# Performance work log

Measured on AMD Instinct MI355X. Metric: run time of the kernel, lower is better.

The kernel has to match this reference:

```python
import jax, jax.numpy as jnp
import numpy as np

T, B, D = 2048, 4, 1024

def setup_inputs() -> dict:
    key = jax.random.key(0)
    ks = jax.random.split(key, 4)
    return {
        "query": jax.random.normal(ks[0], (T, B, D), jnp.float32),
        "input_feature": jax.random.normal(ks[1], (T, B, D), jnp.float32),
        "in_proj_weight": jax.random.normal(ks[2], (2 * D, D), jnp.float32) * (D ** -0.5),
        "in_proj_bias": jnp.zeros((2 * D,), jnp.float32),
        "out_proj_weight": jax.random.normal(ks[3], (D, D), jnp.float32) * (D ** -0.5),
        "out_proj_bias": jnp.zeros((D,), jnp.float32),
    }

def reference(query, input_feature, in_proj_weight, in_proj_bias, out_proj_weight, out_proj_bias):
    d = query.shape[-1]
    scaling = d ** -0.5
    # joint KV projection: [T,B,2D], then chunk
    kv = jnp.einsum('tbd,ed->tbe', input_feature, in_proj_weight) + in_proj_bias
    k, v = kv[..., :d], kv[..., d:]
    q = query * scaling
    # attn_weights: [B, T(query), S(key)]
    attn_weights = jnp.einsum('tbd,sbd->bts', q, k)
    attn_weights = jax.nn.softmax(attn_weights.astype(jnp.float32), axis=-1).astype(q.dtype)
    # attn: [B,T,D] -> [T,B,D]
    attn = jnp.einsum('bts,sbd->tbd', attn_weights, v)
    attn = jnp.einsum('tbd,ed->tbe', attn, out_proj_weight) + out_proj_bias
    return attn, attn_weights
```

## Files before the change

### kernel.cpp

```cpp
#include <hip/hip_runtime.h>
#include <hip/hip_bf16.h>
#include <type_traits>

static constexpr int T = 2048;
static constexpr int B = 4;
static constexpr int D = 1024;
static constexpr int E = 2 * D;
static constexpr int M1 = T * B;

typedef __attribute__((ext_vector_type(8))) short short8;
typedef __attribute__((ext_vector_type(4))) float f32x4;

__device__ inline ushort f2bf(float x) {
    __hip_bfloat16 h = __float2bfloat16(x);
    return __builtin_bit_cast(ushort, h);
}

__device__ inline void glds16(const void* g, void* l) {
    __builtin_amdgcn_global_load_lds(
        (const __attribute__((address_space(1))) void*)g,
        (__attribute__((address_space(3))) void*)l, 16, 0, 0);
}

template <typename OT>
__global__ __launch_bounds__(256) void mfma_gemm_nt(
    const ushort* __restrict__ A, const ushort* __restrict__ Bt,
    OT* __restrict__ C, const float* __restrict__ bias,
    int K, int lda, int ldb, int ldc,
    long long aBatch, long long bBatch, long long cBatch, float alpha)
{
    __shared__ ushort As[128 * 64];
    __shared__ ushort Bs[128 * 64];

    const int tid  = threadIdx.x;
    const int lane = tid & 63;
    const int wave = tid >> 6;
    const int wm = (wave & 1) * 64;
    const int wn = (wave >> 1) * 64;

    const int bm = blockIdx.y * 128;
    const int bn = blockIdx.x * 128;
    A  += blockIdx.z * aBatch;
    Bt += blockIdx.z * bBatch;
    C  += blockIdx.z * cBatch;

    f32x4 acc[4][4] = {};

    const int srow  = lane >> 3;
    const int sElem = (((lane & 7) ^ (lane >> 3))) * 8;
    const int rbase = ((lane >> 4) ^ (lane & 7)) * 8;
    const int rxor4 = 4 * 8;

    for (int k0 = 0; k0 < K; k0 += 64) {
        __syncthreads();
#pragma unroll
        for (int j = 0; j < 4; ++j) {
            const int r = wave * 32 + j * 8;
            glds16(Bt + (long long)(bn + r + srow) * ldb + (k0 + sElem),
                   (void*)&Bs[r * 64]);
            glds16(A + (long long)(bm + r + srow) * lda + (k0 + sElem),
                   (void*)&As[r * 64]);
        }
        __syncthreads();

#pragma unroll
        for (int kb = 0; kb < 2; ++kb) {
            const int rElem = rbase ^ (kb ? rxor4 : 0);
            short8 af[4], bf[4];
#pragma unroll
            for (int i = 0; i < 4; ++i) {
                const int m = wm + i * 16 + (lane & 15);
                af[i] = *(const short8*)&As[m * 64 + rElem];
            }
#pragma unroll
            for (int j = 0; j < 4; ++j) {
                const int n = wn + j * 16 + (lane & 15);
                bf[j] = *(const short8*)&Bs[n * 64 + rElem];
            }
#pragma unroll
            for (int i = 0; i < 4; ++i)
#pragma unroll
                for (int j = 0; j < 4; ++j)
                    acc[i][j] = __builtin_amdgcn_mfma_f32_16x16x32_bf16(af[i], bf[j], acc[i][j], 0, 0, 0);
        }
    }

#pragma unroll
    for (int j = 0; j < 4; ++j) {
        const int col = bn + wn + j * 16 + (lane & 15);
        const float bv = bias ? bias[col] : 0.0f;
#pragma unroll
        for (int i = 0; i < 4; ++i) {
            const int row0 = bm + wm + i * 16 + ((lane >> 4) << 2);
#pragma unroll
            for (int r = 0; r < 4; ++r) {
                const float v = acc[i][j][r] * alpha + bv;
                if constexpr (std::is_same<OT, float>::value)
                    C[(long long)(row0 + r) * ldc + col] = v;
                else
                    C[(long long)(row0 + r) * ldc + col] = f2bf(v);
            }
        }
    }
}

__global__ __launch_bounds__(256) void cast_all(
    const float* __restrict__ s0, ushort* __restrict__ d0, int n0,
    const float* __restrict__ s1, ushort* __restrict__ d1, int n1,
    const float* __restrict__ s2, ushort* __restrict__ d2, int n2,
    const float* __restrict__ s3, ushort* __restrict__ d3, int n3)
{
    int blk = blockIdx.x;
    const float* s; ushort* d;
    if (blk < n0) { s = s0; d = d0; }
    else if ((blk -= n0) < n1) { s = s1; d = d1; }
    else if ((blk -= n1) < n2) { s = s2; d = d2; }
    else { blk -= n2; s = s3; d = d3; }
    const int i = blk * 256 + threadIdx.x;
    const float4 v = ((const float4*)s)[i];
    ushort4 o;
    o.x = f2bf(v.x); o.y = f2bf(v.y); o.z = f2bf(v.z); o.w = f2bf(v.w);
    ((ushort4*)d)[i] = o;
}

__global__ __launch_bounds__(256) void transpose_v(const ushort* __restrict__ kv,
                                                   ushort* __restrict__ vt)
{
    __shared__ ushort tile[64][65];
    const int s0 = blockIdx.x * 64, d0 = blockIdx.y * 64, b = blockIdx.z;
    const int t = threadIdx.x;
    const int dl = (t & 15) * 4, sl = t >> 4;
#pragma unroll
    for (int p = 0; p < 4; ++p) {
        const int s = sl + p * 16;
        const ushort4 v = *(const ushort4*)&kv[((long long)(s0 + s) * B + b) * E + D + d0 + dl];
        tile[s][dl + 0] = v.x; tile[s][dl + 1] = v.y;
        tile[s][dl + 2] = v.z; tile[s][dl + 3] = v.w;
    }
    __syncthreads();
    const int dl2 = t >> 4, sl2 = (t & 15) * 4;
#pragma unroll
    for (int p = 0; p < 4; ++p) {
        const int d = dl2 + p * 16;
        ushort4 o;
        o.x = tile[sl2 + 0][d]; o.y = tile[sl2 + 1][d];
        o.z = tile[sl2 + 2][d]; o.w = tile[sl2 + 3][d];
        *(ushort4*)&vt[(long long)b * D * T + (long long)(d0 + d) * T + s0 + sl2] = o;
    }
}

__global__ __launch_bounds__(256) void softmax_kernel(float* __restrict__ W,
                                                      ushort* __restrict__ Pbf)
{
    const long long row = blockIdx.x;
    float* p = W + row * (long long)T;
    ushort* pb = Pbf + row * (long long)T;
    const int tid = threadIdx.x;

    float4 v0 = ((const float4*)p)[tid];
    float4 v1 = ((const float4*)p)[tid + 256];

    float m = fmaxf(fmaxf(fmaxf(v0.x, v0.y), fmaxf(v0.z, v0.w)),
                    fmaxf(fmaxf(v1.x, v1.y), fmaxf(v1.z, v1.w)));
#pragma unroll
    for (int off = 1; off < 64; off <<= 1) m = fmaxf(m, __shfl_xor(m, off));

    __shared__ float red[4];
    const int wid = tid >> 6, lane = tid & 63;
    if (lane == 0) red[wid] = m;
    __syncthreads();
    m = fmaxf(fmaxf(red[0], red[1]), fmaxf(red[2], red[3]));
    __syncthreads();

    v0.x = expf(v0.x - m); v0.y = expf(v0.y - m);
    v0.z = expf(v0.z - m); v0.w = expf(v0.w - m);
    v1.x = expf(v1.x - m); v1.y = expf(v1.y - m);
    v1.z = expf(v1.z - m); v1.w = expf(v1.w - m);

    float s = v0.x + v0.y + v0.z + v0.w + v1.x + v1.y + v1.z + v1.w;
#pragma unroll
    for (int off = 1; off < 64; off <<= 1) s += __shfl_xor(s, off);
    if (lane == 0) red[wid] = s;
    __syncthreads();
    s = red[0] + red[1] + red[2] + red[3];

    const float inv = 1.0f / s;
    v0.x *= inv; v0.y *= inv; v0.z *= inv; v0.w *= inv;
    v1.x *= inv; v1.y *= inv; v1.z *= inv; v1.w *= inv;

    ((float4*)p)[tid] = v0;
    ((float4*)p)[tid + 256] = v1;

    ushort4 o0, o1;
    o0.x = f2bf(v0.x); o0.y = f2bf(v0.y); o0.z = f2bf(v0.z); o0.w = f2bf(v0.w);
    o1.x = f2bf(v1.x); o1.y = f2bf(v1.y); o1.z = f2bf(v1.z); o1.w = f2bf(v1.w);
    ((ushort4*)pb)[tid] = o0;
    ((ushort4*)pb)[tid + 256] = o1;
}

extern "C" void kernel_launch(void* const* d_in, const int* in_sizes, int n_in,
                              void* d_out, int out_size, void* d_ws, size_t ws_size,
                              hipStream_t stream)
{
    const float* query = (const float*)d_in[0];
    const float* x     = (const float*)d_in[1];
    const float* w_in  = (const float*)d_in[2];
    const float* b_in  = (const float*)d_in[3];
    const float* w_out = (const float*)d_in[4];
    const float* b_out = (const float*)d_in[5];

    float* out_attn = (float*)d_out;
    float* out_w    = out_attn + (long long)T * B * D;

    char* ws = (char*)d_ws;
    ushort* xbf  = (ushort*)(ws);
    ushort* amid = (ushort*)(ws);
    ushort* qbf  = (ushort*)(ws + (16ll << 20));
    ushort* wibf = (ushort*)(ws + (32ll << 20));
    ushort* wobf = (ushort*)(ws + (36ll << 20));
    ushort* kv   = (ushort*)(ws + (38ll << 20));
    ushort* Pbf  = (ushort*)(ws + (38ll << 20));
    ushort* vt   = (ushort*)(ws + (70ll << 20));

    cast_all<<<dim3(8192 + 2048 + 8192 + 1024), 256, 0, stream>>>(
        x, xbf, 8192, w_in, wibf, 2048, query, qbf, 8192, w_out, wobf, 1024);

    mfma_gemm_nt<ushort><<<dim3(E / 128, M1 / 128, 1), 256, 0, stream>>>(
        xbf, wibf, kv, b_in, D, D, D, E, 0, 0, 0, 1.0f);

    transpose_v<<<dim3(T / 64, D / 64, B), 256, 0, stream>>>(kv, vt);

    mfma_gemm_nt<float><<<dim3(T / 128, T / 128, B), 256, 0, stream>>>(
        qbf, kv, out_w, nullptr, D, B * D, B * E, T,
        (long long)D, (long long)E, (long long)T * T, 0.03125f);

    softmax_kernel<<<dim3(B * T), 256, 0, stream>>>(out_w, Pbf);

    mfma_gemm_nt<ushort><<<dim3(D / 128, T / 128, B), 256, 0, stream>>>(
        Pbf, vt, amid, nullptr, T, T, T, B * D,
        (long long)T * T, (long long)D * T, (long long)D, 1.0f);

    mfma_gemm_nt<float><<<dim3(D / 128, M1 / 128, 1), 256, 0, stream>>>(
        amid, wobf, out_attn, b_out, D, D, D, D, 0, 0, 0, 1.0f);
}
```

Before: 354.4 us.

## Replace 128x128 GEMM with double-buffered 256x256 tile kernel using 8 waves

All four GEMMs now use a new kernel with 256x256 output tiles, 512 threads, and 128KB of dynamic LDS. The LDS is double-buffered, and the next K-tile's A and B loads are issued in quarters interleaved with the MFMA work. Explicit barriers, vmcnt waits and s_setprio around the MFMA blocks are meant to overlap global-to-LDS copies with compute and improve reuse per loaded byte. The cost is fewer blocks, e.g. only 64 for the 2048-wide GEMMs and 32 for PV, which risks underfilling the CUs. The hand-tuned wait counts are also fragile, and the address math is now 32-bit.

```diff
diff --git a/kernel.cpp b/kernel.cpp
--- a/kernel.cpp
+++ b/kernel.cpp
@@ -22,75 +22,138 @@
         (__attribute__((address_space(3))) void*)l, 16, 0, 0);
 }
 
+
+#define STAGE_A(p_, half_, t_) do {                                            \
+    const int k0_ = (t_) << 6;                                                 \
+    _Pragma("unroll")                                                          \
+    for (int i_ = 0; i_ < 2; ++i_) {                                           \
+        const int r_ = (half_) * 128 + i_ * 64 + wave * 8;                     \
+        glds16(A + ((bm + r_ + srow) * lda + k0_ + sElem),                     \
+               (void*)&As[(p_) * 16384 + r_ * 64]);                            \
+    } } while (0)
+
+#define STAGE_B(p_, half_, t_) do {                                            \
+    const int k0_ = (t_) << 6;                                                 \
+    _Pragma("unroll")                                                          \
+    for (int i_ = 0; i_ < 2; ++i_) {                                           \
+        const int r_ = (half_) * 128 + i_ * 64 + wave * 8;                     \
+        glds16(Bt + ((bn + r_ + srow) * ldb + k0_ + sElem),                    \
+               (void*)&Bs[(p_) * 16384 + r_ * 64]);                            \
+    } } while (0)
+
+#define READ_A(MOFF)                                                           \
+    _Pragma("unroll") for (int i = 0; i < 4; ++i) {                            \
+        const int m_ = wm + (MOFF) + i * 16 + l15;                             \
+        af_[i][0] = *(const short8*)&as_[m_ * 64 + rbase];                     \
+        af_[i][1] = *(const short8*)&as_[m_ * 64 + (rbase ^ 32)];              \
+    }
+
+#define READ_B(JOFF)                                                           \
+    _Pragma("unroll") for (int j = 0; j < 2; ++j) {                            \
+        const int n_ = wn + ((JOFF) + j) * 16 + l15;                           \
+        bf_[(JOFF) + j][0] = *(const short8*)&bs_[n_ * 64 + rbase];            \
+        bf_[(JOFF) + j][1] = *(const short8*)&bs_[n_ * 64 + (rbase ^ 32)];     \
+    }
+
+#define MFMA_QUAD(IOFF, JOFF)                                                  \
+    _Pragma("unroll") for (int i = 0; i < 4; ++i)                              \
+    _Pragma("unroll") for (int j = 0; j < 2; ++j)                              \
+    _Pragma("unroll") for (int kb = 0; kb < 2; ++kb)                           \
+        acc[(IOFF) + i][(JOFF) + j] = __builtin_amdgcn_mfma_f32_16x16x32_bf16( \
+            af_[i][kb], bf_[(JOFF) + j][kb], acc[(IOFF) + i][(JOFF) + j], 0, 0, 0)
+
+#define TILE(P_, TT_) {                                                        \
+    const ushort* as_ = As + (P_) * 16384;                                     \
+    const ushort* bs_ = Bs + (P_) * 16384;                                     \
+    short8 af_[4][2], bf_[4][2];                                               \
+                                                                  \
+    READ_A(0)                                                                  \
+    READ_B(0)                                                                  \
+    if ((TT_) + 1 < NT) { STAGE_B((P_) ^ 1, 0, (TT_) + 1); }                   \
+    __builtin_amdgcn_s_barrier();                                              \
+    __builtin_amdgcn_s_setprio(1);                                             \
+    MFMA_QUAD(0, 0);                                                           \
+    __builtin_amdgcn_s_setprio(0);                                             \
+    __builtin_amdgcn_s_barrier();                                              \
+                                                                  \
+    READ_B(2)                                                                  \
+    if ((TT_) + 1 < NT) { STAGE_B((P_) ^ 1, 1, (TT_) + 1); }                   \
+    __builtin_amdgcn_s_barrier();                                              \
+    __builtin_amdgcn_s_setprio(1);                                             \
+    MFMA_QUAD(0, 2);                                                           \
+    __builtin_amdgcn_s_setprio(0);                                             \
+    __builtin_amdgcn_s_barrier();                                              \
+                                                                  \
+    READ_A(64)                                                                 \
+    __builtin_amdgcn_s_barrier();                                              \
+    __builtin_amdgcn_s_setprio(1);                                             \
+    MFMA_QUAD(4, 0);                                                           \
+    __builtin_amdgcn_s_setprio(0);                                             \
+    __builtin_amdgcn_s_barrier();                                              \
+                                                                  \
+    if ((TT_) + 2 < NT) { STAGE_A((P_), 0, (TT_) + 2); STAGE_A((P_), 1, (TT_) + 2); } \
+    __builtin_amdgcn_s_barrier();                                              \
+    __builtin_amdgcn_s_setprio(1);                                             \
+    MFMA_QUAD(4, 2);                                                           \
+    __builtin_amdgcn_s_setprio(0);                                             \
+    if ((TT_) + 2 < NT)      { asm volatile("s_waitcnt vmcnt(4)" ::: "memory"); } \
+    else if ((TT_) + 1 < NT) { asm volatile("s_waitcnt vmcnt(0)" ::: "memory"); } \
+    __builtin_amdgcn_s_barrier();                                              \
+}
+
 template <typename OT>
-__global__ __launch_bounds__(256) void mfma_gemm_nt(
+__global__ __launch_bounds__(512, 2) void gemm256(
     const ushort* __restrict__ A, const ushort* __restrict__ Bt,
     OT* __restrict__ C, const float* __restrict__ bias,
     int K, int lda, int ldb, int ldc,
     long long aBatch, long long bBatch, long long cBatch, float alpha)
 {
-    __shared__ ushort As[128 * 64];
-    __shared__ ushort Bs[128 * 64];
+    extern __shared__ ushort lds[];
+    ushort* As = lds;
+    ushort* Bs = lds + 2 * 16384;
 
     const int tid  = threadIdx.x;
     const int lane = tid & 63;
     const int wave = tid >> 6;
-    const int wm = (wave & 1) * 64;
-    const int wn = (wave >> 1) * 64;
-
-    const int bm = blockIdx.y * 128;
-    const int bn = blockIdx.x * 128;
+    const int wm = (wave >> 2) * 128;
+    const int wn = (wave & 3) * 64;
+    const int l15 = lane & 15;
+
+    const int bm = blockIdx.y * 256;
+    const int bn = blockIdx.x * 256;
     A  += blockIdx.z * aBatch;
     Bt += blockIdx.z * bBatch;
     C  += blockIdx.z * cBatch;
 
-    f32x4 acc[4][4] = {};
+    f32x4 acc[8][4] = {};
 
     const int srow  = lane >> 3;
-    const int sElem = (((lane & 7) ^ (lane >> 3))) * 8;
+    const int sElem = ((lane & 7) ^ (lane >> 3)) * 8;
     const int rbase = ((lane >> 4) ^ (lane & 7)) * 8;
-    const int rxor4 = 4 * 8;
-
-    for (int k0 = 0; k0 < K; k0 += 64) {
-        __syncthreads();
-#pragma unroll
-        for (int j = 0; j < 4; ++j) {
-            const int r = wave * 32 + j * 8;
-            glds16(Bt + (long long)(bn + r + srow) * ldb + (k0 + sElem),
-                   (void*)&Bs[r * 64]);
-            glds16(A + (long long)(bm + r + srow) * lda + (k0 + sElem),
-                   (void*)&As[r * 64]);
-        }
-        __syncthreads();
-
-#pragma unroll
-        for (int kb = 0; kb < 2; ++kb) {
-            const int rElem = rbase ^ (kb ? rxor4 : 0);
-            short8 af[4], bf[4];
-#pragma unroll
-            for (int i = 0; i < 4; ++i) {
-                const int m = wm + i * 16 + (lane & 15);
-                af[i] = *(const short8*)&As[m * 64 + rElem];
-            }
-#pragma unroll
-            for (int j = 0; j < 4; ++j) {
-                const int n = wn + j * 16 + (lane & 15);
-                bf[j] = *(const short8*)&Bs[n * 64 + rElem];
-            }
-#pragma unroll
-            for (int i = 0; i < 4; ++i)
-#pragma unroll
-                for (int j = 0; j < 4; ++j)
-                    acc[i][j] = __builtin_amdgcn_mfma_f32_16x16x32_bf16(af[i], bf[j], acc[i][j], 0, 0, 0);
-        }
+
+    const int NT = K >> 6;
+
+    STAGE_A(0, 0, 0); STAGE_A(0, 1, 0);
+    STAGE_B(0, 0, 0); STAGE_B(0, 1, 0);
+    if (NT > 1) {
+        STAGE_A(1, 0, 1); STAGE_A(1, 1, 1);
+        asm volatile("s_waitcnt vmcnt(4)" ::: "memory");
+    } else {
+        asm volatile("s_waitcnt vmcnt(0)" ::: "memory");
+    }
+    __builtin_amdgcn_s_barrier();
+
+    for (int t = 0; t < NT; t += 2) {
+        TILE(0, t)
+        TILE(1, t + 1)
     }
 
 #pragma unroll
     for (int j = 0; j < 4; ++j) {
-        const int col = bn + wn + j * 16 + (lane & 15);
+        const int col = bn + wn + j * 16 + l15;
         const float bv = bias ? bias[col] : 0.0f;
 #pragma unroll
-        for (int i = 0; i < 4; ++i) {
+        for (int i = 0; i < 8; ++i) {
             const int row0 = bm + wm + i * 16 + ((lane >> 4) << 2);
 #pragma unroll
             for (int r = 0; r < 4; ++r) {
@@ -103,6 +166,13 @@
         }
     }
 }
+
+#undef TILE
+#undef MFMA_QUAD
+#undef READ_A
+#undef READ_B
+#undef STAGE_A
+#undef STAGE_B
 
 __global__ __launch_bounds__(256) void cast_all(
     const float* __restrict__ s0, ushort* __restrict__ d0, int n0,
@@ -222,24 +292,33 @@
     ushort* Pbf  = (ushort*)(ws + (38ll << 20));
     ushort* vt   = (ushort*)(ws + (70ll << 20));
 
+    static bool attr_done = false;
+    if (!attr_done) {
+        (void)hipFuncSetAttribute(reinterpret_cast<const void*>(&gemm256<ushort>),
+                                  hipFuncAttributeMaxDynamicSharedMemorySize, 131072);
+        (void)hipFuncSetAttribute(reinterpret_cast<const void*>(&gemm256<float>),
+                                  hipFuncAttributeMaxDynamicSharedMemorySize, 131072);
+        attr_done = true;
+    }
+
     cast_all<<<dim3(8192 + 2048 + 8192 + 1024), 256, 0, stream>>>(
         x, xbf, 8192, w_in, wibf, 2048, query, qbf, 8192, w_out, wobf, 1024);
 
-    mfma_gemm_nt<ushort><<<dim3(E / 128, M1 / 128, 1), 256, 0, stream>>>(
+    gemm256<ushort><<<dim3(E / 256, M1 / 256, 1), 512, 131072, stream>>>(
         xbf, wibf, kv, b_in, D, D, D, E, 0, 0, 0, 1.0f);
 
     transpose_v<<<dim3(T / 64, D / 64, B), 256, 0, stream>>>(kv, vt);
 
-    mfma_gemm_nt<float><<<dim3(T / 128, T / 128, B), 256, 0, stream>>>(
+    gemm256<float><<<dim3(T / 256, T / 256, B), 512, 131072, stream>>>(
         qbf, kv, out_w, nullptr, D, B * D, B * E, T,
         (long long)D, (long long)E, (long long)T * T, 0.03125f);
 
     softmax_kernel<<<dim3(B * T), 256, 0, stream>>>(out_w, Pbf);
 
-    mfma_gemm_nt<ushort><<<dim3(D / 128, T / 128, B), 256, 0, stream>>>(
+    gemm256<ushort><<<dim3(D / 256, T / 256, B), 512, 131072, stream>>>(
         Pbf, vt, amid, nullptr, T, T, T, B * D,
         (long long)T * T, (long long)D * T, (long long)D, 1.0f);
 
-    mfma_gemm_nt<float><<<dim3(D / 128, M1 / 128, 1), 256, 0, stream>>>(
+    gemm256<float><<<dim3(D / 256, M1 / 256, 1), 512, 131072, stream>>>(
         amid, wobf, out_attn, b_out, D, D, D, D, 0, 0, 0, 1.0f);
 }
```

Measured after the change: 381.6 us. 1.08x slower.

## Add pipelined 256x256 double-buffered GEMM with XCD swizzle for KV and QK

Applied to the files above, without the earlier changes.

Introduces a 512-thread 256x256-tile GEMM that double-buffers LDS with direct global-to-LDS loads issued between MFMA quads, using barriers and setprio to overlap loads with compute. It is used for the KV projection and the QK^T score GEMM. A block-index swizzle that groups tiles by XCD is also added to both GEMM kernels. The goal is better data reuse and less load latency exposure, at the cost of 128KB of dynamic LDS and lower occupancy. The swizzle hardcodes gridDim.x == 8, which holds for all current launches.

```diff
diff --git a/kernel.cpp b/kernel.cpp
--- a/kernel.cpp
+++ b/kernel.cpp
@@ -20,6 +20,13 @@
     __builtin_amdgcn_global_load_lds(
         (const __attribute__((address_space(1))) void*)g,
         (__attribute__((address_space(3))) void*)l, 16, 0, 0);
+}
+
+__device__ inline void xcd_swizzle(int& bn_i, int& bm_i) {
+    int id = blockIdx.y * 8 + blockIdx.x;
+    id = (id & 7) * gridDim.y + (id >> 3);
+    bn_i = id & 7;
+    bm_i = id >> 3;
 }
 
 template <typename OT>
@@ -38,8 +45,10 @@
     const int wm = (wave & 1) * 64;
     const int wn = (wave >> 1) * 64;
 
-    const int bm = blockIdx.y * 128;
-    const int bn = blockIdx.x * 128;
+    int bn_i, bm_i;
+    xcd_swizzle(bn_i, bm_i);
+    const int bm = bm_i * 128;
+    const int bn = bn_i * 128;
     A  += blockIdx.z * aBatch;
     Bt += blockIdx.z * bBatch;
     C  += blockIdx.z * cBatch;
@@ -103,6 +112,160 @@
         }
     }
 }
+
+
+#define STAGE_A(p_, half_, t_) do {                                           \
+    const int k0_ = (t_) << 6;                                                \
+    _Pragma("unroll")                                                         \
+    for (int i_ = 0; i_ < 2; ++i_) {                                          \
+        const int r_ = (half_) * 128 + i_ * 64 + wave * 8;                    \
+        glds16(A + ((bm + r_ + srow) * lda + k0_ + sElem),                    \
+               (void*)&As[(p_) * 16384 + r_ * 64]);                           \
+    } } while (0)
+
+#define STAGE_B(p_, half_, t_) do {                                           \
+    const int k0_ = (t_) << 6;                                                \
+    _Pragma("unroll")                                                         \
+    for (int i_ = 0; i_ < 2; ++i_) {                                          \
+        const int r_ = (half_) * 128 + i_ * 64 + wave * 8;                    \
+        glds16(Bt + ((bn + r_ + srow) * ldb + k0_ + sElem),                   \
+               (void*)&Bs[(p_) * 16384 + r_ * 64]);                           \
+    } } while (0)
+
+#define READ_A(MOFF)                                                          \
+    _Pragma("unroll") for (int i = 0; i < 4; ++i) {                           \
+        const int m_ = wm + (MOFF) + i * 16 + l15;                            \
+        af_[i][0] = *(const short8*)&as_[m_ * 64 + rbase];                    \
+        af_[i][1] = *(const short8*)&as_[m_ * 64 + (rbase ^ 32)];             \
+    }
+
+#define READ_B(JOFF)                                                          \
+    _Pragma("unroll") for (int j = 0; j < 2; ++j) {                           \
+        const int n_ = wn + ((JOFF) + j) * 16 + l15;                          \
+        bf_[(JOFF) + j][0] = *(const short8*)&bs_[n_ * 64 + rbase];           \
+        bf_[(JOFF) + j][1] = *(const short8*)&bs_[n_ * 64 + (rbase ^ 32)];    \
+    }
+
+#define MFMA_QUAD(IOFF, JOFF)                                                 \
+    _Pragma("unroll") for (int i = 0; i < 4; ++i)                             \
+    _Pragma("unroll") for (int j = 0; j < 2; ++j)                             \
+    _Pragma("unroll") for (int kb = 0; kb < 2; ++kb)                          \
+        acc[(IOFF) + i][(JOFF) + j] = __builtin_amdgcn_mfma_f32_16x16x32_bf16(\
+            af_[i][kb], bf_[(JOFF) + j][kb], acc[(IOFF) + i][(JOFF) + j], 0, 0, 0)
+
+#define TILE(P_, TT_) {                                                       \
+    const ushort* as_ = As + (P_) * 16384;                                    \
+    const ushort* bs_ = Bs + (P_) * 16384;                                    \
+    short8 af_[4][2], bf_[4][2];                                              \
+                                                                 \
+    READ_A(0)                                                                 \
+    READ_B(0)                                                                 \
+    if ((TT_) + 1 < NT) { STAGE_B((P_) ^ 1, 0, (TT_) + 1); }                  \
+    __builtin_amdgcn_s_barrier();                                             \
+    __builtin_amdgcn_s_setprio(1);                                            \
+    MFMA_QUAD(0, 0);                                                          \
+    __builtin_amdgcn_s_setprio(0);                                            \
+    __builtin_amdgcn_s_barrier();                                             \
+                                                                 \
+    READ_B(2)                                                                 \
+    if ((TT_) + 1 < NT) { STAGE_B((P_) ^ 1, 1, (TT_) + 1); }                  \
+    __builtin_amdgcn_s_barrier();                                             \
+    __builtin_amdgcn_s_setprio(1);                                            \
+    MFMA_QUAD(0, 2);                                                          \
+    __builtin_amdgcn_s_setprio(0);                                            \
+    __builtin_amdgcn_s_barrier();                                             \
+                                                                 \
+    READ_A(64)                                                                \
+    __builtin_amdgcn_s_barrier();                                             \
+    __builtin_amdgcn_s_setprio(1);                                            \
+    MFMA_QUAD(4, 0);                                                          \
+    __builtin_amdgcn_s_setprio(0);                                            \
+    __builtin_amdgcn_s_barrier();                                             \
+                                                                 \
+    if ((TT_) + 2 < NT) { STAGE_A((P_), 0, (TT_) + 2); STAGE_A((P_), 1, (TT_) + 2); } \
+    __builtin_amdgcn_s_barrier();                                             \
+    __builtin_amdgcn_s_setprio(1);                                            \
+    MFMA_QUAD(4, 2);                                                          \
+    __builtin_amdgcn_s_setprio(0);                                            \
+    if ((TT_) + 2 < NT)      { asm volatile("s_waitcnt vmcnt(4)" ::: "memory"); } \
+    else if ((TT_) + 1 < NT) { asm volatile("s_waitcnt vmcnt(0)" ::: "memory"); } \
+    __builtin_amdgcn_s_barrier();                                             \
+}
+
+template <typename OT>
+__global__ __launch_bounds__(512, 2) void gemm256(
+    const ushort* __restrict__ A, const ushort* __restrict__ Bt,
+    OT* __restrict__ C, const float* __restrict__ bias,
+    int K, int lda, int ldb, int ldc,
+    long long aBatch, long long bBatch, long long cBatch, float alpha)
+{
+    extern __shared__ ushort lds[];
+    ushort* As = lds;
+    ushort* Bs = lds + 2 * 16384;
+
+    const int tid  = threadIdx.x;
+    const int lane = tid & 63;
+    const int wave = tid >> 6;
+    const int wm = (wave >> 2) * 128;
+    const int wn = (wave & 3) * 64;
+    const int l15 = lane & 15;
+
+    int bn_i, bm_i;
+    xcd_swizzle(bn_i, bm_i);
+    const int bm = bm_i * 256;
+    const int bn = bn_i * 256;
+    A  += blockIdx.z * aBatch;
+    Bt += blockIdx.z * bBatch;
+    C  += blockIdx.z * cBatch;
+
+    f32x4 acc[8][4] = {};
+
+    const int srow  = lane >> 3;
+    const int sElem = ((lane & 7) ^ (lane >> 3)) * 8;
+    const int rbase = ((lane >> 4) ^ (lane & 7)) * 8;
+
+    const int NT = K >> 6;
+
+    STAGE_A(0, 0, 0); STAGE_A(0, 1, 0);
+    STAGE_B(0, 0, 0); STAGE_B(0, 1, 0);
+    if (NT > 1) {
+        STAGE_A(1, 0, 1); STAGE_A(1, 1, 1);
+        asm volatile("s_waitcnt vmcnt(4)" ::: "memory");
+    } else {
+        asm volatile("s_waitcnt vmcnt(0)" ::: "memory");
+    }
+    __builtin_amdgcn_s_barrier();
+
+    for (int t = 0; t < NT; t += 2) {
+        TILE(0, t)
+        TILE(1, t + 1)
+    }
+
+#pragma unroll
+    for (int j = 0; j < 4; ++j) {
+        const int col = bn + wn + j * 16 + l15;
+        const float bv = bias ? bias[col] : 0.0f;
+#pragma unroll
+        for (int i = 0; i < 8; ++i) {
+            const int row0 = bm + wm + i * 16 + ((lane >> 4) << 2);
+#pragma unroll
+            for (int r = 0; r < 4; ++r) {
+                const float v = acc[i][j][r] * alpha + bv;
+                if constexpr (std::is_same<OT, float>::value)
+                    C[(long long)(row0 + r) * ldc + col] = v;
+                else
+                    C[(long long)(row0 + r) * ldc + col] = f2bf(v);
+            }
+        }
+    }
+}
+
+#undef TILE
+#undef MFMA_QUAD
+#undef READ_A
+#undef READ_B
+#undef STAGE_A
+#undef STAGE_B
 
 __global__ __launch_bounds__(256) void cast_all(
     const float* __restrict__ s0, ushort* __restrict__ d0, int n0,
@@ -222,15 +385,24 @@
     ushort* Pbf  = (ushort*)(ws + (38ll << 20));
     ushort* vt   = (ushort*)(ws + (70ll << 20));
 
+    static bool attr_done = false;
+    if (!attr_done) {
+        (void)hipFuncSetAttribute(reinterpret_cast<const void*>(&gemm256<ushort>),
+                                  hipFuncAttributeMaxDynamicSharedMemorySize, 131072);
+        (void)hipFuncSetAttribute(reinterpret_cast<const void*>(&gemm256<float>),
+                                  hipFuncAttributeMaxDynamicSharedMemorySize, 131072);
+        attr_done = true;
+    }
+
     cast_all<<<dim3(8192 + 2048 + 8192 + 1024), 256, 0, stream>>>(
         x, xbf, 8192, w_in, wibf, 2048, query, qbf, 8192, w_out, wobf, 1024);
 
-    mfma_gemm_nt<ushort><<<dim3(E / 128, M1 / 128, 1), 256, 0, stream>>>(
+    gemm256<ushort><<<dim3(E / 256, M1 / 256, 1), 512, 131072, stream>>>(
         xbf, wibf, kv, b_in, D, D, D, E, 0, 0, 0, 1.0f);
 
     transpose_v<<<dim3(T / 64, D / 64, B), 256, 0, stream>>>(kv, vt);
 
-    mfma_gemm_nt<float><<<dim3(T / 128, T / 128, B), 256, 0, stream>>>(
+    gemm256<float><<<dim3(T / 256, T / 256, B), 512, 131072, stream>>>(
         qbf, kv, out_w, nullptr, D, B * D, B * E, T,
         (long long)D, (long long)E, (long long)T * T, 0.03125f);
 
```

After: 351.2 us, median of 2. No clear change (-0.9%).

## Fuse the whole pipeline into one persistent cooperative kernel with grid syncs

Applied to the files above, without the earlier changes.

Replaces the seven separate launches with a single cooperative persistent kernel that runs cast, KV projection, QK^T, V transpose, softmax, PV and output projection as phases separated by grid.sync. GEMM tiles are remapped with an 8-way interleave, also applied to the fallback launches, to improve L2 locality. The V transpose is overlapped with the QK^T phase without an extra barrier. The goal is to remove launch overhead and inter-kernel gaps, at the cost of grid-wide barriers and possibly lower occupancy from forcing persistent blocks.

```diff
diff --git a/kernel.cpp b/kernel.cpp
--- a/kernel.cpp
+++ b/kernel.cpp
@@ -1,4 +1,5 @@
 #include <hip/hip_runtime.h>
+#include <hip/hip_cooperative_groups.h>
 #include <hip/hip_bf16.h>
 #include <type_traits>
 
@@ -23,26 +24,19 @@
 }
 
 template <typename OT>
-__global__ __launch_bounds__(256) void mfma_gemm_nt(
+__device__ __forceinline__ void gemm_body(char* __restrict__ smem,
     const ushort* __restrict__ A, const ushort* __restrict__ Bt,
     OT* __restrict__ C, const float* __restrict__ bias,
-    int K, int lda, int ldb, int ldc,
-    long long aBatch, long long bBatch, long long cBatch, float alpha)
-{
-    __shared__ ushort As[128 * 64];
-    __shared__ ushort Bs[128 * 64];
+    int K, int lda, int ldb, int ldc, float alpha, int bm, int bn)
+{
+    ushort* As = (ushort*)smem;
+    ushort* Bs = (ushort*)(smem + 16384);
 
     const int tid  = threadIdx.x;
     const int lane = tid & 63;
     const int wave = tid >> 6;
     const int wm = (wave & 1) * 64;
     const int wn = (wave >> 1) * 64;
-
-    const int bm = blockIdx.y * 128;
-    const int bn = blockIdx.x * 128;
-    A  += blockIdx.z * aBatch;
-    Bt += blockIdx.z * bBatch;
-    C  += blockIdx.z * cBatch;
 
     f32x4 acc[4][4] = {};
 
@@ -84,6 +78,7 @@
                     acc[i][j] = __builtin_amdgcn_mfma_f32_16x16x32_bf16(af[i], bf[j], acc[i][j], 0, 0, 0);
         }
     }
+    __syncthreads();
 
 #pragma unroll
     for (int j = 0; j < 4; ++j) {
@@ -104,6 +99,154 @@
     }
 }
 
+__device__ __forceinline__ void cast_blk(const float* __restrict__ s,
+                                         ushort* __restrict__ d, int blk) {
+    const int i = blk * 256 + threadIdx.x;
+    const float4 v = ((const float4*)s)[i];
+    ushort4 o;
+    o.x = f2bf(v.x); o.y = f2bf(v.y); o.z = f2bf(v.z); o.w = f2bf(v.w);
+    ((ushort4*)d)[i] = o;
+}
+
+__device__ __forceinline__ void transpose_body(char* __restrict__ smem,
+                                               const ushort* __restrict__ kv,
+                                               ushort* __restrict__ vt,
+                                               int s0, int d0, int b) {
+    typedef ushort row65[65];
+    row65* tile = (row65*)smem;
+    const int t = threadIdx.x;
+    __syncthreads();
+    const int dl = (t & 15) * 4, sl = t >> 4;
+#pragma unroll
+    for (int p = 0; p < 4; ++p) {
+        const int s = sl + p * 16;
+        const ushort4 v = *(const ushort4*)&kv[((long long)(s0 + s) * B + b) * E + D + d0 + dl];
+        tile[s][dl + 0] = v.x; tile[s][dl + 1] = v.y;
+        tile[s][dl + 2] = v.z; tile[s][dl + 3] = v.w;
+    }
+    __syncthreads();
+    const int dl2 = t >> 4, sl2 = (t & 15) * 4;
+#pragma unroll
+    for (int p = 0; p < 4; ++p) {
+        const int d = dl2 + p * 16;
+        ushort4 o;
+        o.x = tile[sl2 + 0][d]; o.y = tile[sl2 + 1][d];
+        o.z = tile[sl2 + 2][d]; o.w = tile[sl2 + 3][d];
+        *(ushort4*)&vt[(long long)b * D * T + (long long)(d0 + d) * T + s0 + sl2] = o;
+    }
+}
+
+__device__ __forceinline__ void softmax_body(char* __restrict__ smem,
+                                             float* __restrict__ W,
+                                             ushort* __restrict__ Pbf,
+                                             long long row) {
+    float* red = (float*)smem;
+    float* p  = W + row * (long long)T;
+    ushort* pb = Pbf + row * (long long)T;
+    const int tid = threadIdx.x;
+    __syncthreads();
+
+    float4 v0 = ((const float4*)p)[tid];
+    float4 v1 = ((const float4*)p)[tid + 256];
+
+    float m = fmaxf(fmaxf(fmaxf(v0.x, v0.y), fmaxf(v0.z, v0.w)),
+                    fmaxf(fmaxf(v1.x, v1.y), fmaxf(v1.z, v1.w)));
+#pragma unroll
+    for (int off = 1; off < 64; off <<= 1) m = fmaxf(m, __shfl_xor(m, off));
+
+    const int wid = tid >> 6, lane = tid & 63;
+    if (lane == 0) red[wid] = m;
+    __syncthreads();
+    m = fmaxf(fmaxf(red[0], red[1]), fmaxf(red[2], red[3]));
+    __syncthreads();
+
+    v0.x = expf(v0.x - m); v0.y = expf(v0.y - m);
+    v0.z = expf(v0.z - m); v0.w = expf(v0.w - m);
+    v1.x = expf(v1.x - m); v1.y = expf(v1.y - m);
+    v1.z = expf(v1.z - m); v1.w = expf(v1.w - m);
+
+    float s = v0.x + v0.y + v0.z + v0.w + v1.x + v1.y + v1.z + v1.w;
+#pragma unroll
+    for (int off = 1; off < 64; off <<= 1) s += __shfl_xor(s, off);
+    if (lane == 0) red[wid] = s;
+    __syncthreads();
+    s = red[0] + red[1] + red[2] + red[3];
+
+    const float inv = 1.0f / s;
+    v0.x *= inv; v0.y *= inv; v0.z *= inv; v0.w *= inv;
+    v1.x *= inv; v1.y *= inv; v1.z *= inv; v1.w *= inv;
+
+    ((float4*)p)[tid] = v0;
+    ((float4*)p)[tid + 256] = v1;
+
+    ushort4 o0, o1;
+    o0.x = f2bf(v0.x); o0.y = f2bf(v0.y); o0.z = f2bf(v0.z); o0.w = f2bf(v0.w);
+    o1.x = f2bf(v1.x); o1.y = f2bf(v1.y); o1.z = f2bf(v1.z); o1.w = f2bf(v1.w);
+    ((ushort4*)pb)[tid] = o0;
+    ((ushort4*)pb)[tid + 256] = o1;
+}
+
+__global__ __launch_bounds__(256, 4) void mega(
+    const float* __restrict__ query, const float* __restrict__ x,
+    const float* __restrict__ w_in, const float* __restrict__ b_in,
+    const float* __restrict__ w_out, const float* __restrict__ b_out,
+    float* __restrict__ out_attn, float* __restrict__ out_w,
+    ushort* xbf, ushort* qbf, ushort* wibf, ushort* wobf,
+    ushort* kv, ushort* Pbf, ushort* vt, ushort* amid)
+{
+    __shared__ __align__(16) char smem[32768];
+    cooperative_groups::grid_group grid = cooperative_groups::this_grid();
+    const int bid = blockIdx.x, gsz = gridDim.x;
+
+    for (int i = bid; i < 8192; i += gsz) cast_blk(x, xbf, i);
+    for (int i = bid; i < 2048; i += gsz) cast_blk(w_in, wibf, i);
+    for (int i = bid; i < 8192; i += gsz) cast_blk(query, qbf, i);
+    for (int i = bid; i < 1024; i += gsz) cast_blk(w_out, wobf, i);
+    grid.sync();
+
+    for (int t0 = bid; t0 < 1024; t0 += gsz) {
+        const int tt = (t0 & 7) * 128 + (t0 >> 3);
+        gemm_body<ushort>(smem, xbf, wibf, kv, b_in, D, D, D, E, 1.0f,
+                          (tt >> 4) * 128, (tt & 15) * 128);
+    }
+    grid.sync();
+
+    for (int t0 = bid; t0 < 1024; t0 += gsz) {
+        const int tt = (t0 & 7) * 128 + (t0 >> 3);
+        const int b = tt >> 8, t = tt & 255;
+        gemm_body<float>(smem, qbf + (long long)b * D, kv + (long long)b * E,
+                         out_w + (long long)b * T * T, nullptr,
+                         D, B * D, B * E, T, 0.03125f,
+                         (t >> 4) * 128, (t & 15) * 128);
+    }
+    for (int s = bid; s < 2048; s += gsz) {
+        const int b = s >> 9, idx = s & 511;
+        transpose_body(smem, kv, vt, (idx & 31) * 64, (idx >> 5) * 64, b);
+    }
+    grid.sync();
+
+    for (int r = bid; r < 8192; r += gsz)
+        softmax_body(smem, out_w, Pbf, r);
+    grid.sync();
+
+    for (int t0 = bid; t0 < 512; t0 += gsz) {
+        const int tt = (t0 & 7) * 64 + (t0 >> 3);
+        const int b = tt >> 7, rem = tt & 127;
+        gemm_body<ushort>(smem, Pbf + (long long)b * T * T,
+                          vt + (long long)b * D * T,
+                          amid + (long long)b * D, nullptr,
+                          T, T, T, B * D, 1.0f,
+                          (rem >> 3) * 128, (rem & 7) * 128);
+    }
+    grid.sync();
+
+    for (int t0 = bid; t0 < 512; t0 += gsz) {
+        const int tt = (t0 & 7) * 64 + (t0 >> 3);
+        gemm_body<float>(smem, amid, wobf, out_attn, b_out,
+                         D, D, D, D, 1.0f, (tt >> 3) * 128, (tt & 7) * 128);
+    }
+}
+
 __global__ __launch_bounds__(256) void cast_all(
     const float* __restrict__ s0, ushort* __restrict__ d0, int n0,
     const float* __restrict__ s1, ushort* __restrict__ d1, int n1,
@@ -116,86 +259,39 @@
     else if ((blk -= n0) < n1) { s = s1; d = d1; }
     else if ((blk -= n1) < n2) { s = s2; d = d2; }
     else { blk -= n2; s = s3; d = d3; }
-    const int i = blk * 256 + threadIdx.x;
-    const float4 v = ((const float4*)s)[i];
-    ushort4 o;
-    o.x = f2bf(v.x); o.y = f2bf(v.y); o.z = f2bf(v.z); o.w = f2bf(v.w);
-    ((ushort4*)d)[i] = o;
+    cast_blk(s, d, blk);
+}
+
+template <typename OT>
+__global__ __launch_bounds__(256) void mfma_gemm_nt(
+    const ushort* __restrict__ A, const ushort* __restrict__ Bt,
+    OT* __restrict__ C, const float* __restrict__ bias,
+    int K, int lda, int ldb, int ldc,
+    long long aBatch, long long bBatch, long long cBatch, float alpha)
+{
+    __shared__ __align__(16) char smem[32768];
+    int id = blockIdx.y * gridDim.x + blockIdx.x;
+    const int q = (gridDim.x * gridDim.y) >> 3;
+    id = (id & 7) * q + (id >> 3);
+    const int bm_i = id / gridDim.x;
+    const int bn_i = id - bm_i * gridDim.x;
+    gemm_body<OT>(smem, A + blockIdx.z * aBatch, Bt + blockIdx.z * bBatch,
+                  C + blockIdx.z * cBatch, bias,
+                  K, lda, ldb, ldc, alpha, bm_i * 128, bn_i * 128);
 }
 
 __global__ __launch_bounds__(256) void transpose_v(const ushort* __restrict__ kv,
                                                    ushort* __restrict__ vt)
 {
-    __shared__ ushort tile[64][65];
-    const int s0 = blockIdx.x * 64, d0 = blockIdx.y * 64, b = blockIdx.z;
-    const int t = threadIdx.x;
-    const int dl = (t & 15) * 4, sl = t >> 4;
-#pragma unroll
-    for (int p = 0; p < 4; ++p) {
-        const int s = sl + p * 16;
-        const ushort4 v = *(const ushort4*)&kv[((long long)(s0 + s) * B + b) * E + D + d0 + dl];
-        tile[s][dl + 0] = v.x; tile[s][dl + 1] = v.y;
-        tile[s][dl + 2] = v.z; tile[s][dl + 3] = v.w;
-    }
-    __syncthreads();
-    const int dl2 = t >> 4, sl2 = (t & 15) * 4;
-#pragma unroll
-    for (int p = 0; p < 4; ++p) {
-        const int d = dl2 + p * 16;
-        ushort4 o;
-        o.x = tile[sl2 + 0][d]; o.y = tile[sl2 + 1][d];
-        o.z = tile[sl2 + 2][d]; o.w = tile[sl2 + 3][d];
-        *(ushort4*)&vt[(long long)b * D * T + (long long)(d0 + d) * T + s0 + sl2] = o;
-    }
+    __shared__ __align__(16) char smem[8320];
+    transpose_body(smem, kv, vt, blockIdx.x * 64, blockIdx.y * 64, blockIdx.z);
 }
 
 __global__ __launch_bounds__(256) void softmax_kernel(float* __restrict__ W,
                                                       ushort* __restrict__ Pbf)
 {
-    const long long row = blockIdx.x;
-    float* p = W + row * (long long)T;
-    ushort* pb = Pbf + row * (long long)T;
-    const int tid = threadIdx.x;
-
-    float4 v0 = ((const float4*)p)[tid];
-    float4 v1 = ((const float4*)p)[tid + 256];
-
-    float m = fmaxf(fmaxf(fmaxf(v0.x, v0.y), fmaxf(v0.z, v0.w)),
-                    fmaxf(fmaxf(v1.x, v1.y), fmaxf(v1.z, v1.w)));
-#pragma unroll
-    for (int off = 1; off < 64; off <<= 1) m = fmaxf(m, __shfl_xor(m, off));
-
-    __shared__ float red[4];
-    const int wid = tid >> 6, lane = tid & 63;
-    if (lane == 0) red[wid] = m;
-    __syncthreads();
-    m = fmaxf(fmaxf(red[0], red[1]), fmaxf(red[2], red[3]));
-    __syncthreads();
-
-    v0.x = expf(v0.x - m); v0.y = expf(v0.y - m);
-    v0.z = expf(v0.z - m); v0.w = expf(v0.w - m);
-    v1.x = expf(v1.x - m); v1.y = expf(v1.y - m);
-    v1.z = expf(v1.z - m); v1.w = expf(v1.w - m);
-
-    float s = v0.x + v0.y + v0.z + v0.w + v1.x + v1.y + v1.z + v1.w;
-#pragma unroll
-    for (int off = 1; off < 64; off <<= 1) s += __shfl_xor(s, off);
-    if (lane == 0) red[wid] = s;
-    __syncthreads();
-    s = red[0] + red[1] + red[2] + red[3];
-
-    const float inv = 1.0f / s;
-    v0.x *= inv; v0.y *= inv; v0.z *= inv; v0.w *= inv;
-    v1.x *= inv; v1.y *= inv; v1.z *= inv; v1.w *= inv;
-
-    ((float4*)p)[tid] = v0;
-    ((float4*)p)[tid + 256] = v1;
-
-    ushort4 o0, o1;
-    o0.x = f2bf(v0.x); o0.y = f2bf(v0.y); o0.z = f2bf(v0.z); o0.w = f2bf(v0.w);
-    o1.x = f2bf(v1.x); o1.y = f2bf(v1.y); o1.z = f2bf(v1.z); o1.w = f2bf(v1.w);
-    ((ushort4*)pb)[tid] = o0;
-    ((ushort4*)pb)[tid + 256] = o1;
+    __shared__ __align__(16) char smem[16];
+    softmax_body(smem, W, Pbf, blockIdx.x);
 }
 
 extern "C" void kernel_launch(void* const* d_in, const int* in_sizes, int n_in,
@@ -222,24 +318,43 @@
     ushort* Pbf  = (ushort*)(ws + (38ll << 20));
     ushort* vt   = (ushort*)(ws + (70ll << 20));
 
-    cast_all<<<dim3(8192 + 2048 + 8192 + 1024), 256, 0, stream>>>(
-        x, xbf, 8192, w_in, wibf, 2048, query, qbf, 8192, w_out, wobf, 1024);
-
-    mfma_gemm_nt<ushort><<<dim3(E / 128, M1 / 128, 1), 256, 0, stream>>>(
-        xbf, wibf, kv, b_in, D, D, D, E, 0, 0, 0, 1.0f);
-
-    transpose_v<<<dim3(T / 64, D / 64, B), 256, 0, stream>>>(kv, vt);
-
-    mfma_gemm_nt<float><<<dim3(T / 128, T / 128, B), 256, 0, stream>>>(
-        qbf, kv, out_w, nullptr, D, B * D, B * E, T,
-        (long long)D, (long long)E, (long long)T * T, 0.03125f);
-
-    softmax_kernel<<<dim3(B * T), 256, 0, stream>>>(out_w, Pbf);
-
-    mfma_gemm_nt<ushort><<<dim3(D / 128, T / 128, B), 256, 0, stream>>>(
-        Pbf, vt, amid, nullptr, T, T, T, B * D,
-        (long long)T * T, (long long)D * T, (long long)D, 1.0f);
-
-    mfma_gemm_nt<float><<<dim3(D / 128, M1 / 128, 1), 256, 0, stream>>>(
-        amid, wobf, out_attn, b_out, D, D, D, D, 0, 0, 0, 1.0f);
-}
+    static int gridsz = 0;
+    if (gridsz == 0) {
+        int nb = 0;
+        if (hipOccupancyMaxActiveBlocksPerMultiprocessor(&nb, mega, 256, 0) != hipSuccess || nb <= 0)
+            nb = 3;
+        hipDeviceProp_t prop;
+        int cus = 256;
+        if (hipGetDeviceProperties(&prop, 0) == hipSuccess) cus = prop.multiProcessorCount;
+        gridsz = nb * cus;
+        if (gridsz > 1024) gridsz = 1024;
+        if (gridsz < 64)   gridsz = 64;
+    }
+
+    const float *a0 = query, *a1 = x, *a2 = w_in, *a3 = b_in, *a4 = w_out, *a5 = b_out;
+    float *a6 = out_attn, *a7 = out_w;
+    ushort *a8 = xbf, *a9 = qbf, *a10 = wibf, *a11 = wobf,
+           *a12 = kv, *a13 = Pbf, *a14 = vt, *a15 = amid;
+    void* args[] = {&a0,&a1,&a2,&a3,&a4,&a5,&a6,&a7,
+                    &a8,&a9,&a10,&a11,&a12,&a13,&a14,&a15};
+
+    hipError_t err = hipLaunchCooperativeKernel(
+        mega, dim3(gridsz), dim3(256), args, 0, stream);
+
+    if (err != hipSuccess) {
+        cast_all<<<dim3(8192 + 2048 + 8192 + 1024), 256, 0, stream>>>(
+            x, xbf, 8192, w_in, wibf, 2048, query, qbf, 8192, w_out, wobf, 1024);
+        mfma_gemm_nt<ushort><<<dim3(E / 128, M1 / 128, 1), 256, 0, stream>>>(
+            xbf, wibf, kv, b_in, D, D, D, E, 0, 0, 0, 1.0f);
+        transpose_v<<<dim3(T / 64, D / 64, B), 256, 0, stream>>>(kv, vt);
+        mfma_gemm_nt<float><<<dim3(T / 128, T / 128, B), 256, 0, stream>>>(
+            qbf, kv, out_w, nullptr, D, B * D, B * E, T,
+            (long long)D, (long long)E, (long long)T * T, 0.03125f);
+        softmax_kernel<<<dim3(B * T), 256, 0, stream>>>(out_w, Pbf);
+        mfma_gemm_nt<ushort><<<dim3(D / 128, T / 128, B), 256, 0, stream>>>(
+            Pbf, vt, amid, nullptr, T, T, T, B * D,
+            (long long)T * T, (long long)D * T, (long long)D, 1.0f);
+        mfma_gemm_nt<float><<<dim3(D / 128, M1 / 128, 1), 256, 0, stream>>>(
+            amid, wobf, out_attn, b_out, D, D, D, D, 0, 0, 0, 1.0f);
+    }
+}
```

Result: slower. 677.4 us (+91.1%).
